# Kernel optimization log

Hardware: AMD Instinct MI355X
Metric: run time of the kernel (lower is better)

The kernel has to match this reference:

```python
import jax, jax.numpy as jnp
import numpy as np
import math

B, NQ, NS, K = 4, 4096, 16384, 16
P, IN, D = 3, 128, 256
H = D // 16   # nhead = out_dim // 16 = 16
HD = D // H   # head_dim = 16
RADIUS = 4.0
EPS = 1e-5


def _ln(x, g, b):
    m = jnp.mean(x, -1, keepdims=True)
    v = jnp.mean((x - m) ** 2, -1, keepdims=True)
    return (x - m) / jnp.sqrt(v + EPS) * g + b


def _pos_enc(x, W_pos, b_pos):
    # LearnablePositionalEncoding: cat([x, cos(Linear(2*pi*x))], -1)
    return jnp.concatenate([x, jnp.cos((2.0 * math.pi * x) @ W_pos + b_pos)], axis=-1)


def setup_inputs() -> dict:
    key = jax.random.key(0)
    ks = jax.random.split(key, 24)
    f32 = jnp.float32

    def w(k, shape):
        return jax.random.uniform(k, shape, f32, -1.0, 1.0) / np.float32(np.sqrt(shape[0]))

    inp = {}
    inp['q_pts'] = jax.random.normal(ks[0], (B, NQ, P), f32)
    inp['s_pts'] = jax.random.normal(ks[1], (B, NS, P), f32)
    inp['src_feats'] = jax.random.normal(ks[2], (B, NS, IN), f32)
    inp['query_feats'] = jax.random.normal(ks[3], (B, NQ, IN), f32)
    # shared proj (in_dim != out_dim, skip_dim=None -> skip_proj is the same Linear)
    inp['W_proj'] = w(ks[4], (IN, D)); inp['b_proj'] = jnp.zeros((D,), f32)
    # positional encoding Linear(p_dim, out_dim - p_dim)
    inp['W_pos'] = w(ks[5], (P, D - P)); inp['b_pos'] = jnp.zeros((D - P,), f32)
    # TransformerDecoderLayer (norm_first) params
    inp['ln1_g'] = jnp.ones((D,), f32); inp['ln1_b'] = jnp.zeros((D,), f32)
    inp['sa_Wv'] = w(ks[6], (D, D)); inp['sa_bv'] = jnp.zeros((D,), f32)
    inp['sa_Wo'] = w(ks[7], (D, D)); inp['sa_bo'] = jnp.zeros((D,), f32)
    inp['ln2_g'] = jnp.ones((D,), f32); inp['ln2_b'] = jnp.zeros((D,), f32)
    inp['ca_Wq'] = w(ks[8], (D, D)); inp['ca_bq'] = jnp.zeros((D,), f32)
    inp['ca_Wk'] = w(ks[9], (D, D)); inp['ca_bk'] = jnp.zeros((D,), f32)
    inp['ca_Wv'] = w(ks[10], (D, D)); inp['ca_bv'] = jnp.zeros((D,), f32)
    inp['ca_Wo'] = w(ks[11], (D, D)); inp['ca_bo'] = jnp.zeros((D,), f32)
    inp['ln3_g'] = jnp.ones((D,), f32); inp['ln3_b'] = jnp.zeros((D,), f32)
    inp['W1'] = w(ks[12], (D, D)); inp['b1'] = jnp.zeros((D,), f32)
    inp['W2'] = w(ks[13], (D, D)); inp['b2'] = jnp.zeros((D,), f32)
    inp['neighb_inds'] = jax.random.randint(ks[14], (B, NQ, K), 0, NS)
    return inp


def reference(q_pts, s_pts, src_feats, query_feats, W_proj, b_proj, W_pos, b_pos,
              ln1_g, ln1_b, sa_Wv, sa_bv, sa_Wo, sa_bo, ln2_g, ln2_b,
              ca_Wq, ca_bq, ca_Wk, ca_bk, ca_Wv, ca_bv, ca_Wo, ca_bo,
              ln3_g, ln3_b, W1, b1, W2, b2, neighb_inds):
    # append shadow point at 1e6 with zero feature row
    s_pts_ = jnp.concatenate([s_pts, jnp.full_like(s_pts[:, :1, :], 1e6)], axis=1)   # [B,NS+1,P]
    src_ = jnp.concatenate([src_feats, jnp.zeros_like(src_feats[:, :1, :])], axis=1)  # [B,NS+1,IN]
    src_p = src_ @ W_proj + b_proj            # proj(src_feats)  [B,NS+1,D]
    qf = query_feats @ W_proj + b_proj        # skip_proj == proj (skip_dim=None)
    inds = neighb_inds % (NS + 1)
    flat = inds.reshape(B, -1, 1)             # [B, NQ*K, 1]
    neighbors = jnp.take_along_axis(s_pts_, jnp.broadcast_to(flat, (B, NQ * K, P)), axis=1).reshape(B, NQ, K, P)
    neighb_x = jnp.take_along_axis(src_p, jnp.broadcast_to(flat, (B, NQ * K, D)), axis=1).reshape(B, NQ, K, D)
    neighbors = neighbors - q_pts[:, :, None, :]
    neighb_x = neighb_x + _pos_enc(neighbors / RADIUS, W_pos, b_pos)
    query_x = qf + _pos_enc(jnp.zeros_like(q_pts), W_pos, b_pos)
    mask = jnp.linalg.norm(neighbors, axis=-1) > RADIUS   # [B,NQ,K], True = invalid key

    x = query_x   # [B,NQ,D]: a length-1 target sequence per query point
    # --- self-attention block (seq len 1 -> softmax == 1 -> only V/O projections matter) ---
    h = _ln(x, ln1_g, ln1_b)
    x = x + (h @ sa_Wv + sa_bv) @ sa_Wo + sa_bo
    # --- cross-attention to K gathered neighbors ---
    h = _ln(x, ln2_g, ln2_b)
    q = (h @ ca_Wq + ca_bq).reshape(B, NQ, H, HD)
    kk = (neighb_x @ ca_Wk + ca_bk).reshape(B, NQ, K, H, HD)
    vv = (neighb_x @ ca_Wv + ca_bv).reshape(B, NQ, K, H, HD)
    scores = jnp.einsum('bnhd,bnkhd->bnhk', q, kk) / np.float32(np.sqrt(HD))
    scores = jnp.where(mask[:, :, None, :], jnp.float32(-1e9), scores)
    att = jax.nn.softmax(scores, axis=-1)
    ctx = jnp.einsum('bnhk,bnkhd->bnhd', att, vv).reshape(B, NQ, D)
    x = x + ctx @ ca_Wo + ca_bo
    # --- feed-forward (dim_feedforward == d_model, relu) ---
    h = _ln(x, ln3_g, ln3_b)
    x = x + jax.nn.relu(h @ W1 + b1) @ W2 + b2
    # original zeroes any NaNs (fully-masked rows); shapes chosen so this is a no-op
    return jnp.nan_to_num(x)
```

## Files before the change

### kernel.cpp

```cpp
#include <hip/hip_runtime.h>
#include <hip/hip_bf16.h>
#include <math.h>
#include <stdint.h>

typedef __attribute__((ext_vector_type(8))) short short8;
typedef __attribute__((ext_vector_type(4))) float floatx4;

#define DEVI __device__ __forceinline__

DEVI float b2f(unsigned short u) {
    union { unsigned int i; float f; } v; v.i = ((unsigned int)u) << 16; return v.f;
}
DEVI unsigned short f2b(float f) {
    unsigned int x = __float_as_uint(f);
    unsigned int r = (x + 0x7fffu + ((x >> 16) & 1u)) >> 16;
    return (unsigned short)r;
}

#define GLD16(gp, lp)                                                            \
    __builtin_amdgcn_global_load_lds(                                            \
        (__attribute__((address_space(1))) unsigned int*)(gp),                   \
        (__attribute__((address_space(3))) unsigned int*)(lp), 16, 0, 0)

static constexpr int NQ = 4096, NS = 16384;
static constexpr int NROW_Q = 4 * NQ;
static constexpr int NROW_S = 4 * NS;
static constexpr float INV2PI = 0.15915494309189535f;

__global__ void k_prep(const float* Wproj, const float* saWv, const float* saWo,
                       const float* caWq, const float* caWk, const float* caWv,
                       const float* caWo, const float* W1, const float* W2,
                       const float* b_pos,
                       unsigned short* wTproj, unsigned short* wTsaWv, unsigned short* wTsaWo,
                       unsigned short* wTcaWq, unsigned short* wTkv, unsigned short* wTcaWo,
                       unsigned short* wTW1, unsigned short* wTW2, float* penc0)
{
    int z = blockIdx.z;
    if (z == 9) {
        if (blockIdx.x == 0 && blockIdx.y == 0) {
            int c = threadIdx.y * 16 + threadIdx.x;
            float v = 0.f;
            if (c >= 3) {
                float rev = b_pos[c - 3] * INV2PI;
                rev -= floorf(rev);
                v = __builtin_amdgcn_cosf(rev);
            }
            penc0[c] = v;
        }
        return;
    }
    int n = blockIdx.x * 16 + threadIdx.x;
    int k = blockIdx.y * 16 + threadIdx.y;
    const float* src; unsigned short* dst; int K = 256;
    switch (z) {
        case 0: src = Wproj; dst = wTproj; K = 128; break;
        case 1: src = saWv;  dst = wTsaWv; break;
        case 2: src = saWo;  dst = wTsaWo; break;
        case 3: src = caWq;  dst = wTcaWq; break;
        case 4: src = caWk;  dst = wTkv;   break;
        case 5: src = caWv;  dst = wTkv + 256 * 256; break;
        case 6: src = caWo;  dst = wTcaWo; break;
        case 7: src = W1;    dst = wTW1;   break;
        default: src = W2;   dst = wTW2;   break;
    }
    if (k < K) dst[(size_t)n * K + k] = f2b(src[(size_t)k * 256 + n]);
}

__global__ void k_cvt(const float* in, unsigned short* out, int n4)
{
    int i = blockIdx.x * blockDim.x + threadIdx.x;
    int stride = gridDim.x * blockDim.x;
    for (; i < n4; i += stride) {
        float4 v = ((const float4*)in)[i];
        unsigned long long p =
              (unsigned long long)f2b(v.x)
            | ((unsigned long long)f2b(v.y) << 16)
            | ((unsigned long long)f2b(v.z) << 32)
            | ((unsigned long long)f2b(v.w) << 48);
        ((unsigned long long*)out)[i] = p;
    }
}

template<int EPI>
__global__ __launch_bounds__(256, 2)
void k_gemm(const unsigned short* A, const unsigned short* BT, const float* bias,
            const float* extra, void* outp, int M, int N, int K)
{
    __shared__ alignas(16) unsigned short lA[128 * 64];
    __shared__ alignas(16) unsigned short lB[64 * 64];
    const int tid = threadIdx.x;
    const int wave = tid >> 6, lane = tid & 63;
    const int m0 = blockIdx.x * 128, n0 = blockIdx.y * 64;
    const int wm = (wave >> 1) * 64, wn = (wave & 1) * 32;
    floatx4 acc[4][2] = {};

    for (int kt = 0; kt < K; kt += 64) {
        __syncthreads();
        #pragma unroll
        for (int c = 0; c < 4; ++c) {
            int o = (tid + c * 256) * 16;
            int row = o >> 7, inner = o & 127;
            int srk = inner ^ ((row & 7) << 4);
            GLD16((const char*)A + ((size_t)(m0 + row) * K + kt) * 2 + srk, (char*)lA + o);
        }
        #pragma unroll
        for (int c = 0; c < 2; ++c) {
            int o = (tid + c * 256) * 16;
            int row = o >> 7, inner = o & 127;
            int srk = inner ^ ((row & 7) << 4);
            GLD16((const char*)BT + ((size_t)(n0 + row) * K + kt) * 2 + srk, (char*)lB + o);
        }
        __syncthreads();
        #pragma unroll
        for (int kc = 0; kc < 2; ++kc) {
            const int kb = kc * 64 + ((lane >> 4) << 4);
            short8 bf[2];
            #pragma unroll
            for (int nf = 0; nf < 2; ++nf) {
                int nn = wn + nf * 16 + (lane & 15);
                bf[nf] = *(const short8*)((const char*)lB + nn * 128 + (kb ^ ((nn & 7) << 4)));
            }
            #pragma unroll
            for (int mf = 0; mf < 4; ++mf) {
                int rr = wm + mf * 16 + (lane & 15);
                short8 af = *(const short8*)((const char*)lA + rr * 128 + (kb ^ ((rr & 7) << 4)));
                acc[mf][0] = __builtin_amdgcn_mfma_f32_16x16x32_bf16(af, bf[0], acc[mf][0], 0, 0, 0);
                acc[mf][1] = __builtin_amdgcn_mfma_f32_16x16x32_bf16(af, bf[1], acc[mf][1], 0, 0, 0);
            }
        }
    }
    #pragma unroll
    for (int mf = 0; mf < 4; ++mf)
        #pragma unroll
        for (int nf = 0; nf < 2; ++nf)
            #pragma unroll
            for (int r = 0; r < 4; ++r) {
                int row = m0 + wm + mf * 16 + ((lane >> 4) << 2) + r;
                int col = n0 + wn + nf * 16 + (lane & 15);
                float v = acc[mf][nf][r] + bias[col];
                if (EPI == 2) v += extra[col];
                if (EPI == 3 || EPI == 4) v += extra[(size_t)row * N + col];
                if (EPI == 1) v = fmaxf(v, 0.f);
                if (EPI == 4) {
                    if (isnan(v)) v = 0.f;
                    else if (isinf(v)) v = v > 0.f ? 3.402823466e38f : -3.402823466e38f;
                }
                if (EPI == 0 || EPI == 1)
                    ((unsigned short*)outp)[(size_t)row * N + col] = f2b(v);
                else
                    ((float*)outp)[(size_t)row * N + col] = v;
            }
}

__global__ __launch_bounds__(256, 2)
void k_ln(const float* x, const float* g, const float* b, unsigned short* out)
{
    int row = blockIdx.x * 4 + (threadIdx.x >> 6);
    int lane = threadIdx.x & 63;
    const float* xr = x + (size_t)row * 256;
    float4 v = ((const float4*)xr)[lane];
    float s = v.x + v.y + v.z + v.w;
    #pragma unroll
    for (int t = 32; t >= 1; t >>= 1) s += __shfl_xor(s, t, 64);
    float mean = s * (1.f / 256.f);
    float d0 = v.x - mean, d1 = v.y - mean, d2 = v.z - mean, d3 = v.w - mean;
    float q = d0 * d0 + d1 * d1 + d2 * d2 + d3 * d3;
    #pragma unroll
    for (int t = 32; t >= 1; t >>= 1) q += __shfl_xor(q, t, 64);
    float inv = 1.0f / sqrtf(q * (1.f / 256.f) + 1e-5f);
    int c = lane * 4;
    unsigned long long p =
          (unsigned long long)f2b(d0 * inv * g[c] + b[c])
        | ((unsigned long long)f2b(d1 * inv * g[c + 1] + b[c + 1]) << 16)
        | ((unsigned long long)f2b(d2 * inv * g[c + 2] + b[c + 2]) << 32)
        | ((unsigned long long)f2b(d3 * inv * g[c + 3] + b[c + 3]) << 48);
    ((unsigned long long*)(out + (size_t)row * 256))[lane] = p;
}

__global__ __launch_bounds__(512, 2)
void k_attn(const unsigned short* srcp, const unsigned short* qb, const int* inds,
            const float* s_pts, const float* q_pts, const float* W_pos, const float* b_pos,
            const unsigned short* wTkv, const float* bv, unsigned short* ctx)
{
    __shared__ alignas(1024) char lds[151552];
    unsigned short* nx  = (unsigned short*)lds;
    unsigned short* kkL = (unsigned short*)(lds + 67584);
    unsigned short* vvL = (unsigned short*)lds;
    char* bst0 = lds + 67584;
    char* bst1 = lds + 135168;
    const int tid = threadIdx.x, wave = tid >> 6, lane = tid & 63;
    const int qbase = blockIdx.x * 8;

    {
        int r = tid >> 2, sub = tid & 3;
        int qi = qbase + (r >> 4);
        int bb = qi >> 12;
        int k = r & 15;
        int raw = inds[((size_t)qi << 4) + k];
        int idx = raw % (NS + 1); if (idx < 0) idx += NS + 1;
        float px = q_pts[(size_t)qi * 3], py = q_pts[(size_t)qi * 3 + 1], pz = q_pts[(size_t)qi * 3 + 2];
        bool shadow = (idx == NS);
        float sx, sy, sz;
        const unsigned short* srow = srcp;
        if (shadow) { sx = sy = sz = 1e6f; }
        else {
            const float* sp = s_pts + ((size_t)bb * NS + idx) * 3;
            sx = sp[0]; sy = sp[1]; sz = sp[2];
            srow = srcp + ((size_t)bb * NS + idx) * 256;
        }
        float tx = (sx - px) * 0.25f, ty = (sy - py) * 0.25f, tz = (sz - pz) * 0.25f;
        const int c0 = sub * 64;
        for (int cc = 0; cc < 64; cc += 8) {
            short8 sv = {0, 0, 0, 0, 0, 0, 0, 0};
            if (!shadow) sv = *(const short8*)(srow + c0 + cc);
            short8 vals;
            #pragma unroll
            for (int j = 0; j < 8; ++j) {
                int c = c0 + cc + j;
                float pe;
                if (c == 0) pe = tx;
                else if (c == 1) pe = ty;
                else if (c == 2) pe = tz;
                else {
                    int jj = c - 3;
                    float rev = fmaf(tx, W_pos[jj],
                                fmaf(ty, W_pos[253 + jj],
                                fmaf(tz, W_pos[506 + jj], b_pos[jj] * INV2PI)));
                    rev -= floorf(rev);
                    pe = __builtin_amdgcn_cosf(rev);
                }
                float sval = shadow ? 0.f : b2f((unsigned short)sv[j]);
                vals[j] = (short)f2b(sval + pe);
            }
            int byte = (c0 + cc) * 2;
            *(short8*)((char*)nx + r * 512 + (byte ^ ((r & 7) << 4))) = vals;
        }
    }
    __syncthreads();

    const int wm = (wave >> 2) * 64;
    const int wn = (wave & 3) * 64;
    #pragma unroll 1
    for (int pass = 0; pass < 2; ++pass) {
        char* bs = pass ? bst1 : bst0;
        floatx4 acc[4][4] = {};
        #pragma unroll 1
        for (int kt = 0; kt < 8; ++kt) {
            __syncthreads();
            #pragma unroll
            for (int c = 0; c < 2; ++c) {
                int o = (tid + c * 512) * 16;
                int row = o >> 6, inner = o & 63;
                int srk = inner ^ ((row & 3) << 4);
                GLD16((const char*)wTkv + ((size_t)(pass * 256 + row)) * 512 + kt * 64 + srk, bs + o);
            }
            __syncthreads();
            const int kb = (lane >> 4) << 4;
            short8 bfr[4];
            #pragma unroll
            for (int nf = 0; nf < 4; ++nf) {
                int nn = wn + nf * 16 + (lane & 15);
                bfr[nf] = *(const short8*)(bs + nn * 64 + (kb ^ ((nn & 3) << 4)));
            }
            #pragma unroll
            for (int mf = 0; mf < 4; ++mf) {
                int rr = wm + mf * 16 + (lane & 15);
                short8 af = *(const short8*)((const char*)nx + rr * 512 + ((kt * 64 + kb) ^ ((rr & 7) << 4)));
                #pragma unroll
                for (int nf = 0; nf < 4; ++nf)
                    acc[mf][nf] = __builtin_amdgcn_mfma_f32_16x16x32_bf16(af, bfr[nf], acc[mf][nf], 0, 0, 0);
            }
        }
        __syncthreads();
        unsigned short* dst = pass ? vvL : kkL;
        #pragma unroll
        for (int mf = 0; mf < 4; ++mf)
            #pragma unroll
            for (int nf = 0; nf < 4; ++nf)
                #pragma unroll
                for (int r = 0; r < 4; ++r) {
                    int row = wm + mf * 16 + ((lane >> 4) << 2) + r;
                    int col = wn + nf * 16 + (lane & 15);
                    dst[row * 264 + col] = f2b(acc[mf][nf][r]);
                }
    }
    __syncthreads();

    {
        int qi = qbase + wave;
        int bb = qi >> 12;
        int s = lane & 15, g = lane >> 4;
        int raw = inds[((size_t)qi << 4) + s];
        int idx = raw % (NS + 1); if (idx < 0) idx += NS + 1;
        float px = q_pts[(size_t)qi * 3], py = q_pts[(size_t)qi * 3 + 1], pz = q_pts[(size_t)qi * 3 + 2];
        float sx, sy, sz;
        if (idx == NS) { sx = sy = sz = 1e6f; }
        else { const float* sp = s_pts + ((size_t)bb * NS + idx) * 3; sx = sp[0]; sy = sp[1]; sz = sp[2]; }
        float dx = sx - px, dy = sy - py, dz = sz - pz;
        bool masked = sqrtf(dx * dx + dy * dy + dz * dz) > 4.0f;

        const unsigned short* qrow = qb + (size_t)qi * 256;
        float attv[4];
        #pragma unroll
        for (int i = 0; i < 4; ++i) {
            int h = g * 4 + i;
            const unsigned short* kr = kkL + ((size_t)(wave * 16 + s)) * 264 + h * 16;
            short8 k0 = *(const short8*)kr;
            short8 k1 = *(const short8*)(kr + 8);
            short8 q0 = *(const short8*)(qrow + h * 16);
            short8 q1 = *(const short8*)(qrow + h * 16 + 8);
            float sc = 0.f;
            #pragma unroll
            for (int d = 0; d < 8; ++d) {
                sc = fmaf(b2f((unsigned short)q0[d]), b2f((unsigned short)k0[d]), sc);
                sc = fmaf(b2f((unsigned short)q1[d]), b2f((unsigned short)k1[d]), sc);
            }
            sc *= 0.25f;
            if (masked) sc = -1e9f;
            float m = sc;
            #pragma unroll
            for (int t = 8; t >= 1; t >>= 1) m = fmaxf(m, __shfl_xor(m, t, 16));
            float p = __expf(sc - m);
            float su = p;
            #pragma unroll
            for (int t = 8; t >= 1; t >>= 1) su += __shfl_xor(su, t, 16);
            attv[i] = p / su;
        }
        int d = s;
        #pragma unroll
        for (int i = 0; i < 4; ++i) {
            int h = g * 4 + i;
            float o = 0.f;
            #pragma unroll
            for (int k2 = 0; k2 < 16; ++k2) {
                float a = __shfl(attv[i], (lane & 48) + k2, 64);
                o = fmaf(a, b2f(vvL[((size_t)(wave * 16 + k2)) * 264 + h * 16 + d]), o);
            }
            o += bv[h * 16 + d];
            ctx[(size_t)qi * 256 + h * 16 + d] = f2b(o);
        }
    }
}

extern "C" void kernel_launch(void* const* d_in, const int* in_sizes, int n_in,
                              void* d_out, int out_size, void* d_ws, size_t ws_size,
                              hipStream_t stream)
{
    const float* q_pts   = (const float*)d_in[0];
    const float* s_pts   = (const float*)d_in[1];
    const float* src_f   = (const float*)d_in[2];
    const float* query_f = (const float*)d_in[3];
    const float* W_proj  = (const float*)d_in[4];
    const float* b_proj  = (const float*)d_in[5];
    const float* W_pos   = (const float*)d_in[6];
    const float* b_pos   = (const float*)d_in[7];
    const float* ln1_g   = (const float*)d_in[8];
    const float* ln1_b   = (const float*)d_in[9];
    const float* sa_Wv   = (const float*)d_in[10];
    const float* sa_bv   = (const float*)d_in[11];
    const float* sa_Wo   = (const float*)d_in[12];
    const float* sa_bo   = (const float*)d_in[13];
    const float* ln2_g   = (const float*)d_in[14];
    const float* ln2_b   = (const float*)d_in[15];
    const float* ca_Wq   = (const float*)d_in[16];
    const float* ca_bq   = (const float*)d_in[17];
    const float* ca_Wk   = (const float*)d_in[18];
    const float* ca_Wv   = (const float*)d_in[20];
    const float* ca_bv   = (const float*)d_in[21];
    const float* ca_Wo   = (const float*)d_in[22];
    const float* ca_bo   = (const float*)d_in[23];
    const float* ln3_g   = (const float*)d_in[24];
    const float* ln3_b   = (const float*)d_in[25];
    const float* W1      = (const float*)d_in[26];
    const float* b1      = (const float*)d_in[27];
    const float* W2      = (const float*)d_in[28];
    const float* b2      = (const float*)d_in[29];
    const int*   inds    = (const int*)d_in[30];

    char* ws = (char*)d_ws;
    size_t off = 0;
    auto alloc = [&](size_t bytes) { char* p = ws + off; off += (bytes + 1023) & ~(size_t)1023; return p; };

    unsigned short* wTproj = (unsigned short*)alloc(256 * 128 * 2);
    unsigned short* wTsaWv = (unsigned short*)alloc(256 * 256 * 2);
    unsigned short* wTsaWo = (unsigned short*)alloc(256 * 256 * 2);
    unsigned short* wTcaWq = (unsigned short*)alloc(256 * 256 * 2);
    unsigned short* wTkv   = (unsigned short*)alloc(512 * 256 * 2);
    unsigned short* wTcaWo = (unsigned short*)alloc(256 * 256 * 2);
    unsigned short* wTW1   = (unsigned short*)alloc(256 * 256 * 2);
    unsigned short* wTW2   = (unsigned short*)alloc(256 * 256 * 2);
    float*          penc0  = (float*)alloc(256 * 4);
    unsigned short* srcb   = (unsigned short*)alloc((size_t)NROW_S * 128 * 2);
    unsigned short* qfb    = (unsigned short*)alloc((size_t)NROW_Q * 128 * 2);
    unsigned short* srcp   = (unsigned short*)alloc((size_t)NROW_S * 256 * 2);
    float*          qx     = (float*)alloc((size_t)NROW_Q * 256 * 4);
    unsigned short* hbuf   = (unsigned short*)alloc((size_t)NROW_Q * 256 * 2);
    unsigned short* tbuf   = (unsigned short*)alloc((size_t)NROW_Q * 256 * 2);
    float*          xbuf   = (float*)alloc((size_t)NROW_Q * 256 * 4);
    unsigned short* qbuf   = (unsigned short*)alloc((size_t)NROW_Q * 256 * 2);
    unsigned short* ctxbuf = (unsigned short*)alloc((size_t)NROW_Q * 256 * 2);
    float*          x2buf  = (float*)alloc((size_t)NROW_Q * 256 * 4);

    dim3 bl16(16, 16);
    k_prep<<<dim3(16, 16, 10), bl16, 0, stream>>>(
        W_proj, sa_Wv, sa_Wo, ca_Wq, ca_Wk, ca_Wv, ca_Wo, W1, W2, b_pos,
        wTproj, wTsaWv, wTsaWo, wTcaWq, wTkv, wTcaWo, wTW1, wTW2, penc0);

    k_cvt<<<1024, 256, 0, stream>>>(src_f, srcb, NROW_S * 128 / 4);
    k_cvt<<<1024, 256, 0, stream>>>(query_f, qfb, NROW_Q * 128 / 4);

    k_gemm<0><<<dim3(512, 4), 256, 0, stream>>>(srcb, wTproj, b_proj, nullptr, srcp, NROW_S, 256, 128);
    k_gemm<2><<<dim3(128, 4), 256, 0, stream>>>(qfb, wTproj, b_proj, penc0, qx, NROW_Q, 256, 128);

    k_ln<<<4096, 256, 0, stream>>>(qx, ln1_g, ln1_b, hbuf);
    k_gemm<0><<<dim3(128, 4), 256, 0, stream>>>(hbuf, wTsaWv, sa_bv, nullptr, tbuf, NROW_Q, 256, 256);
    k_gemm<3><<<dim3(128, 4), 256, 0, stream>>>(tbuf, wTsaWo, sa_bo, qx, xbuf, NROW_Q, 256, 256);

    k_ln<<<4096, 256, 0, stream>>>(xbuf, ln2_g, ln2_b, hbuf);
    k_gemm<0><<<dim3(128, 4), 256, 0, stream>>>(hbuf, wTcaWq, ca_bq, nullptr, qbuf, NROW_Q, 256, 256);
    k_attn<<<2048, 512, 0, stream>>>(srcp, qbuf, inds, s_pts, q_pts, W_pos, b_pos, wTkv, ca_bv, ctxbuf);
    k_gemm<3><<<dim3(128, 4), 256, 0, stream>>>(ctxbuf, wTcaWo, ca_bo, xbuf, x2buf, NROW_Q, 256, 256);

    k_ln<<<4096, 256, 0, stream>>>(x2buf, ln3_g, ln3_b, hbuf);
    k_gemm<1><<<dim3(128, 4), 256, 0, stream>>>(hbuf, wTW1, b1, nullptr, tbuf, NROW_Q, 256, 256);
    k_gemm<4><<<dim3(128, 4), 256, 0, stream>>>(tbuf, wTW2, b2, x2buf, d_out, NROW_Q, 256, 256);

    (void)in_sizes; (void)n_in; (void)out_size; (void)ws_size;
}
```

Measured before the change: 409.9 us.

## Fuse attention softmax into K/V MFMA registers, drop LDS staging of weights and K/V

```diff
diff --git a/kernel.cpp b/kernel.cpp
--- a/kernel.cpp
+++ b/kernel.cpp
@@ -177,19 +177,17 @@
     ((unsigned long long*)(out + (size_t)row * 256))[lane] = p;
 }
 
-__global__ __launch_bounds__(512, 2)
+__global__ __launch_bounds__(256, 4)
 void k_attn(const unsigned short* srcp, const unsigned short* qb, const int* inds,
             const float* s_pts, const float* q_pts, const float* W_pos, const float* b_pos,
             const unsigned short* wTkv, const float* bv, unsigned short* ctx)
 {
-    __shared__ alignas(1024) char lds[151552];
-    unsigned short* nx  = (unsigned short*)lds;
-    unsigned short* kkL = (unsigned short*)(lds + 67584);
-    unsigned short* vvL = (unsigned short*)lds;
-    char* bst0 = lds + 67584;
-    char* bst1 = lds + 135168;
+    __shared__ alignas(16) unsigned short nx[64 * 256];
+    __shared__ alignas(16) float att_lds[4 * 16 * 16];
+    __shared__ alignas(16) float dist_lds[64];
     const int tid = threadIdx.x, wave = tid >> 6, lane = tid & 63;
-    const int qbase = blockIdx.x * 8;
+    const int qbase = blockIdx.x * 4;
+    const int l15 = lane & 15, lg = lane >> 4;
 
     {
         int r = tid >> 2, sub = tid & 3;
@@ -209,6 +207,7 @@
             srow = srcp + ((size_t)bb * NS + idx) * 256;
         }
         float tx = (sx - px) * 0.25f, ty = (sy - py) * 0.25f, tz = (sz - pz) * 0.25f;
+        if (sub == 0) dist_lds[r] = tx * tx + ty * ty + tz * tz;
         const int c0 = sub * 64;
         for (int cc = 0; cc < 64; cc += 8) {
             short8 sv = {0, 0, 0, 0, 0, 0, 0, 0};
@@ -233,112 +232,121 @@
                 vals[j] = (short)f2b(sval + pe);
             }
             int byte = (c0 + cc) * 2;
-            *(short8*)((char*)nx + r * 512 + (byte ^ ((r & 7) << 4))) = vals;
+            *(short8*)((char*)nx + r * 512 + (byte ^ ((r & 7) << 4)))= vals;
         }
     }
     __syncthreads();
 
-    const int wm = (wave >> 2) * 64;
-    const int wn = (wave & 3) * 64;
-    #pragma unroll 1
-    for (int pass = 0; pass < 2; ++pass) {
-        char* bs = pass ? bst1 : bst0;
-        floatx4 acc[4][4] = {};
-        #pragma unroll 1
-        for (int kt = 0; kt < 8; ++kt) {
-            __syncthreads();
-            #pragma unroll
-            for (int c = 0; c < 2; ++c) {
-                int o = (tid + c * 512) * 16;
-                int row = o >> 6, inner = o & 63;
-                int srk = inner ^ ((row & 3) << 4);
-                GLD16((const char*)wTkv + ((size_t)(pass * 256 + row)) * 512 + kt * 64 + srk, bs + o);
-            }
-            __syncthreads();
-            const int kb = (lane >> 4) << 4;
-            short8 bfr[4];
+    const int wn = wave * 64;
+    floatx4 acc[4][4];
+
+    #pragma unroll
+    for (int mf = 0; mf < 4; ++mf)
+        #pragma unroll
+        for (int nf = 0; nf < 4; ++nf) acc[mf][nf] = floatx4{0.f, 0.f, 0.f, 0.f};
+
+    for (int kt = 0; kt < 8; ++kt) {
+        short8 bfr[4], afr[4];
+        #pragma unroll
+        for (int nf = 0; nf < 4; ++nf) {
+            int nn = wn + nf * 16 + l15;
+            bfr[nf] = *(const short8*)((const char*)wTkv + (size_t)nn * 512 + kt * 64 + (lg << 4));
+        }
+        #pragma unroll
+        for (int mf = 0; mf < 4; ++mf) {
+            int rr = mf * 16 + l15;
+            afr[mf] = *(const short8*)((const char*)nx + rr * 512 + ((kt * 64 + (lg << 4)) ^ ((rr & 7) << 4)));
+        }
+        #pragma unroll
+        for (int mf = 0; mf < 4; ++mf)
+            #pragma unroll
+            for (int nf = 0; nf < 4; ++nf)
+                acc[mf][nf] = __builtin_amdgcn_mfma_f32_16x16x32_bf16(afr[mf], bfr[nf], acc[mf][nf], 0, 0, 0);
+    }
+
+    {
+        float qv[4][4];
+        #pragma unroll
+        for (int mf = 0; mf < 4; ++mf)
+            #pragma unroll
+            for (int nf = 0; nf < 4; ++nf)
+                qv[mf][nf] = b2f(qb[(size_t)(qbase + mf) * 256 + (wave * 4 + nf) * 16 + l15]);
+        #pragma unroll
+        for (int mf = 0; mf < 4; ++mf) {
+            float4 d4 = *(const float4*)&dist_lds[mf * 16 + lg * 4];
+            float dd4[4] = {d4.x, d4.y, d4.z, d4.w};
             #pragma unroll
             for (int nf = 0; nf < 4; ++nf) {
-                int nn = wn + nf * 16 + (lane & 15);
-                bfr[nf] = *(const short8*)(bs + nn * 64 + (kb ^ ((nn & 3) << 4)));
-            }
-            #pragma unroll
-            for (int mf = 0; mf < 4; ++mf) {
-                int rr = wm + mf * 16 + (lane & 15);
-                short8 af = *(const short8*)((const char*)nx + rr * 512 + ((kt * 64 + kb) ^ ((rr & 7) << 4)));
+                float s[4];
                 #pragma unroll
-                for (int nf = 0; nf < 4; ++nf)
-                    acc[mf][nf] = __builtin_amdgcn_mfma_f32_16x16x32_bf16(af, bfr[nf], acc[mf][nf], 0, 0, 0);
-            }
-        }
-        __syncthreads();
-        unsigned short* dst = pass ? vvL : kkL;
+                for (int r = 0; r < 4; ++r) s[r] = acc[mf][nf][r] * qv[mf][nf];
+                #pragma unroll
+                for (int t = 1; t <= 8; t <<= 1)
+                    #pragma unroll
+                    for (int r = 0; r < 4; ++r) s[r] += __shfl_xor(s[r], t);
+                #pragma unroll
+                for (int r = 0; r < 4; ++r)
+                    s[r] = (dd4[r] > 1.0f) ? -1e9f : s[r] * 0.25f;
+                float m = fmaxf(fmaxf(s[0], s[1]), fmaxf(s[2], s[3]));
+                m = fmaxf(m, __shfl_xor(m, 16));
+                m = fmaxf(m, __shfl_xor(m, 32));
+                float p[4], su = 0.f;
+                #pragma unroll
+                for (int r = 0; r < 4; ++r) { p[r] = __expf(s[r] - m); su += p[r]; }
+                su += __shfl_xor(su, 16);
+                su += __shfl_xor(su, 32);
+                float inv = __builtin_amdgcn_rcpf(su);
+                if (l15 == 0) {
+                    float4 a4 = {p[0] * inv, p[1] * inv, p[2] * inv, p[3] * inv};
+                    *(float4*)&att_lds[(mf * 16 + wave * 4 + nf) * 16 + lg * 4] = a4;
+                }
+            }
+        }
+    }
+
+    #pragma unroll
+    for (int mf = 0; mf < 4; ++mf)
+        #pragma unroll
+        for (int nf = 0; nf < 4; ++nf) acc[mf][nf] = floatx4{0.f, 0.f, 0.f, 0.f};
+
+    for (int kt = 0; kt < 8; ++kt) {
+        short8 bfr[4], afr[4];
+        #pragma unroll
+        for (int nf = 0; nf < 4; ++nf) {
+            int nn = 256 + wn + nf * 16 + l15;
+            bfr[nf] = *(const short8*)((const char*)wTkv + (size_t)nn * 512 + kt * 64 + (lg << 4));
+        }
+        #pragma unroll
+        for (int mf = 0; mf < 4; ++mf) {
+            int rr = mf * 16 + l15;
+            afr[mf] = *(const short8*)((const char*)nx + rr * 512 + ((kt * 64 + (lg << 4)) ^ ((rr & 7) << 4)));
+        }
         #pragma unroll
         for (int mf = 0; mf < 4; ++mf)
             #pragma unroll
             for (int nf = 0; nf < 4; ++nf)
-                #pragma unroll
-                for (int r = 0; r < 4; ++r) {
-                    int row = wm + mf * 16 + ((lane >> 4) << 2) + r;
-                    int col = wn + nf * 16 + (lane & 15);
-                    dst[row * 264 + col] = f2b(acc[mf][nf][r]);
-                }
-    }
-    __syncthreads();
+                acc[mf][nf] = __builtin_amdgcn_mfma_f32_16x16x32_bf16(afr[mf], bfr[nf], acc[mf][nf], 0, 0, 0);
+    }
 
     {
-        int qi = qbase + wave;
-        int bb = qi >> 12;
-        int s = lane & 15, g = lane >> 4;
-        int raw = inds[((size_t)qi << 4) + s];
-        int idx = raw % (NS + 1); if (idx < 0) idx += NS + 1;
-        float px = q_pts[(size_t)qi * 3], py = q_pts[(size_t)qi * 3 + 1], pz = q_pts[(size_t)qi * 3 + 2];
-        float sx, sy, sz;
-        if (idx == NS) { sx = sy = sz = 1e6f; }
-        else { const float* sp = s_pts + ((size_t)bb * NS + idx) * 3; sx = sp[0]; sy = sp[1]; sz = sp[2]; }
-        float dx = sx - px, dy = sy - py, dz = sz - pz;
-        bool masked = sqrtf(dx * dx + dy * dy + dz * dz) > 4.0f;
-
-        const unsigned short* qrow = qb + (size_t)qi * 256;
-        float attv[4];
-        #pragma unroll
-        for (int i = 0; i < 4; ++i) {
-            int h = g * 4 + i;
-            const unsigned short* kr = kkL + ((size_t)(wave * 16 + s)) * 264 + h * 16;
-            short8 k0 = *(const short8*)kr;
-            short8 k1 = *(const short8*)(kr + 8);
-            short8 q0 = *(const short8*)(qrow + h * 16);
-            short8 q1 = *(const short8*)(qrow + h * 16 + 8);
-            float sc = 0.f;
-            #pragma unroll
-            for (int d = 0; d < 8; ++d) {
-                sc = fmaf(b2f((unsigned short)q0[d]), b2f((unsigned short)k0[d]), sc);
-                sc = fmaf(b2f((unsigned short)q1[d]), b2f((unsigned short)k1[d]), sc);
-            }
-            sc *= 0.25f;
-            if (masked) sc = -1e9f;
-            float m = sc;
-            #pragma unroll
-            for (int t = 8; t >= 1; t >>= 1) m = fmaxf(m, __shfl_xor(m, t, 16));
-            float p = __expf(sc - m);
-            float su = p;
-            #pragma unroll
-            for (int t = 8; t >= 1; t >>= 1) su += __shfl_xor(su, t, 16);
-            attv[i] = p / su;
-        }
-        int d = s;
-        #pragma unroll
-        for (int i = 0; i < 4; ++i) {
-            int h = g * 4 + i;
-            float o = 0.f;
-            #pragma unroll
-            for (int k2 = 0; k2 < 16; ++k2) {
-                float a = __shfl(attv[i], (lane & 48) + k2, 64);
-                o = fmaf(a, b2f(vvL[((size_t)(wave * 16 + k2)) * 264 + h * 16 + d]), o);
-            }
-            o += bv[h * 16 + d];
-            ctx[(size_t)qi * 256 + h * 16 + d] = f2b(o);
-        }
+        float bvv[4];
+        #pragma unroll
+        for (int nf = 0; nf < 4; ++nf) bvv[nf] = bv[(wave * 4 + nf) * 16 + l15];
+        #pragma unroll
+        for (int mf = 0; mf < 4; ++mf)
+            #pragma unroll
+            for (int nf = 0; nf < 4; ++nf) {
+                float4 a4 = *(const float4*)&att_lds[(mf * 16 + wave * 4 + nf) * 16 + lg * 4];
+                float o = a4.x * acc[mf][nf][0];
+                o = fmaf(a4.y, acc[mf][nf][1], o);
+                o = fmaf(a4.z, acc[mf][nf][2], o);
+                o = fmaf(a4.w, acc[mf][nf][3], o);
+                o += __shfl_xor(o, 16);
+                o += __shfl_xor(o, 32);
+                o += bvv[nf];
+                if (lane < 16)
+                    ctx[(size_t)(qbase + mf) * 256 + (wave * 4 + nf) * 16 + lane] = f2b(o);
+            }
     }
 }
 
@@ -418,7 +426,7 @@
 
     k_ln<<<4096, 256, 0, stream>>>(xbuf, ln2_g, ln2_b, hbuf);
     k_gemm<0><<<dim3(128, 4), 256, 0, stream>>>(hbuf, wTcaWq, ca_bq, nullptr, qbuf, NROW_Q, 256, 256);
-    k_attn<<<2048, 512, 0, stream>>>(srcp, qbuf, inds, s_pts, q_pts, W_pos, b_pos, wTkv, ca_bv, ctxbuf);
+    k_attn<<<4096, 256, 0, stream>>>(srcp, qbuf, inds, s_pts, q_pts, W_pos, b_pos, wTkv, ca_bv, ctxbuf);
     k_gemm<3><<<dim3(128, 4), 256, 0, stream>>>(ctxbuf, wTcaWo, ca_bo, xbuf, x2buf, NROW_Q, 256, 256);
 
     k_ln<<<4096, 256, 0, stream>>>(x2buf, ln3_g, ln3_b, hbuf);
```

Measured after the change: 398.2 us. -2.9%, faster.
